# Kernel optimization log

Hardware: AMD Instinct MI355X
Metric: run time of the kernel (lower is better)

Reference implementation:

```python
import jax, jax.numpy as jnp
import numpy as np

N = 100000
E = 1600000
C_IN = 128
C_HID = 128


def setup_inputs() -> dict:
    key = jax.random.key(0)
    ks = jax.random.split(key, 6)
    x = jax.random.normal(ks[0], (N, C_IN), dtype=jnp.float32)
    edge_index = jax.random.randint(ks[1], (2, E), 0, N, dtype=jnp.int64)
    # GCNConv params: linear weight + bias per layer (glorot-ish scale)
    W1 = jax.random.normal(ks[2], (C_IN, C_HID), dtype=jnp.float32) / np.sqrt(C_IN)
    b1 = jnp.zeros((C_HID,), dtype=jnp.float32)
    W2 = jax.random.normal(ks[3], (C_HID, C_HID), dtype=jnp.float32) / np.sqrt(C_HID)
    b2 = jnp.zeros((C_HID,), dtype=jnp.float32)
    return {"x": x, "edge_index": edge_index, "W1": W1, "b1": b1, "W2": W2, "b2": b2}


def _gcn_conv(x, W, b, src, dst, n_nodes):
    # PyG GCNConv: h = D^{-1/2} (A + I) D^{-1/2} (x W) + b
    h = x @ W  # [N, C_out]
    # add self-loops
    loop = jnp.arange(n_nodes, dtype=src.dtype)
    s = jnp.concatenate([src, loop])
    d = jnp.concatenate([dst, loop])
    ones = jnp.ones(s.shape[0], dtype=h.dtype)
    deg = jax.ops.segment_sum(ones, d, num_segments=n_nodes)  # in-degree incl self-loop
    dinv = jnp.where(deg > 0, jax.lax.rsqrt(deg), 0.0)
    norm = dinv[s] * dinv[d]  # [E+N]
    msg = h[s] * norm[:, None]  # gather + scale
    out = jax.ops.segment_sum(msg, d, num_segments=n_nodes)  # scatter-add
    return out + b


def reference(x, edge_index, W1, b1, W2, b2):
    src, dst = edge_index[0], edge_index[1]
    h = jax.nn.relu(_gcn_conv(x, W1, b1, src, dst, N))
    h = jax.nn.relu(_gcn_conv(h, W2, b2, src, dst, N))
    return h
```

## Files before the change

kernel.cpp:

```cpp
#include <hip/hip_runtime.h>
#include <hip/hip_bf16.h>

#define GCN_N 100000
#define GB1 1563
#define NBUCK 391
#define BCAP 8192
#define KPWG 391

typedef unsigned short u16;
typedef unsigned int u32;
typedef float f32x4 __attribute__((ext_vector_type(4)));
typedef short bf16x8 __attribute__((ext_vector_type(8)));

union v16 { uint4 u; bf16x8 h; };

__device__ inline u16 f2bf(float f) {
    u32 u = __float_as_uint(f);
    return (u16)((u + 0x7fffu + ((u >> 16) & 1u)) >> 16);
}
__device__ inline u32 pack2(float a, float b) {
    return (u32)f2bf(a) | ((u32)f2bf(b) << 16);
}
__device__ inline float bf_lo(u32 u) { return __uint_as_float(u << 16); }
__device__ inline float bf_hi(u32 u) { return __uint_as_float(u & 0xffff0000u); }
__device__ inline u32 scale2(u32 p, float d) {
    return pack2(bf_lo(p) * d, bf_hi(p) * d);
}

__device__ inline void addu8(float* a, float4 v) {
    u32 u;
    u = __float_as_uint(v.x); a[0] += bf_lo(u); a[1] += bf_hi(u);
    u = __float_as_uint(v.y); a[2] += bf_lo(u); a[3] += bf_hi(u);
    u = __float_as_uint(v.z); a[4] += bf_lo(u); a[5] += bf_hi(u);
    u = __float_as_uint(v.w); a[6] += bf_lo(u); a[7] += bf_hi(u);
}
__device__ inline void setu8(float* a, float4 v) {
    u32 u;
    u = __float_as_uint(v.x); a[0] = bf_lo(u); a[1] = bf_hi(u);
    u = __float_as_uint(v.y); a[2] = bf_lo(u); a[3] = bf_hi(u);
    u = __float_as_uint(v.z); a[4] = bf_lo(u); a[5] = bf_hi(u);
    u = __float_as_uint(v.w); a[6] = bf_lo(u); a[7] = bf_hi(u);
}

__device__ inline void mfma16(f32x4& d, uint4 a, uint4 b) {
    v16 av, bv; av.u = a; bv.u = b;
    d = __builtin_amdgcn_mfma_f32_16x16x32_bf16(av.h, bv.h, d, 0, 0, 0);
}

__global__ __launch_bounds__(256) void k_init(int* __restrict__ gcursor,
                                              const float* __restrict__ W1,
                                              const float* __restrict__ W2,
                                              u16* __restrict__ Wt1,
                                              u16* __restrict__ Wt2) {
    if (blockIdx.x == 0) {
        for (int i = threadIdx.x; i < NBUCK; i += 256) gcursor[i] = 0;
        return;
    }
    const float* W = (blockIdx.x == 1) ? W1 : W2;
    u16* Wt = (blockIdx.x == 1) ? Wt1 : Wt2;
    for (int i = threadIdx.x; i < 16384; i += 256) {
        int k = i >> 7, nn = i & 127;
        Wt[nn * 128 + k] = f2bf(W[i]);
    }
}

template<int SCALE>
__device__ __attribute__((always_inline))
inline void gemm_core(const uint4* Xs, const u16* __restrict__ Wt,
                      const float* __restrict__ dinv, u16* __restrict__ H,
                      long long row0, int n) {
    const int t = threadIdx.x;
    const int wid = t >> 6;
    const int l = t & 63, lm = l & 15, lh = l >> 4;
    uint4 a[4];
    const int lrow = wid * 16 + lm;
    #pragma unroll
    for (int kk = 0; kk < 4; ++kk) {
        int byte = (lrow * 256 + kk * 64 + lh * 16) ^ ((lm & 7) << 4);
        a[kk] = Xs[byte >> 4];
    }
    const uint4* wb = (const uint4*)Wt;
    f32x4 acc[8];
    #pragma unroll
    for (int j = 0; j < 8; ++j) acc[j] = (f32x4){0.f, 0.f, 0.f, 0.f};
    #pragma unroll
    for (int j = 0; j < 8; ++j) {
        #pragma unroll
        for (int kk = 0; kk < 4; ++kk) {
            uint4 b = wb[(j * 16 + lm) * 16 + kk * 4 + lh];
            mfma16(acc[j], a[kk], b);
        }
    }
    long long gr0 = row0 + wid * 16 + lh * 4;
    float dv[4];
    #pragma unroll
    for (int r = 0; r < 4; ++r)
        dv[r] = SCALE ? ((gr0 + r < n) ? dinv[gr0 + r] : 0.f) : 1.f;
    #pragma unroll
    for (int j = 0; j < 8; ++j) {
        #pragma unroll
        for (int r = 0; r < 4; ++r) {
            long long grow = gr0 + r;
            if (grow < n)
                H[grow * 128 + j * 16 + lm] =
                    f2bf(SCALE ? acc[j][r] * dv[r] : acc[j][r]);
        }
    }
}

__global__ __launch_bounds__(256) void k_part_gemm1(
        const int* __restrict__ src, const int* __restrict__ dst,
        int* __restrict__ gcursor, u32* __restrict__ part,
        const float* __restrict__ X, const u16* __restrict__ Wt,
        u16* __restrict__ H, int E, int n) {
    __shared__ uint4 Xs[1024];
    if (blockIdx.x < KPWG) {
        int* lhist = (int*)Xs;
        int* lbase = lhist + NBUCK;
        int* lcur  = lbase + NBUCK;
        const int t = threadIdx.x;
        for (int i = t; i < NBUCK; i += 256) { lhist[i] = 0; lcur[i] = 0; }
        __syncthreads();
        const long long e0 = (long long)blockIdx.x * 4096;
        #pragma unroll
        for (int i = 0; i < 16; ++i) {
            long long e = e0 + i * 256 + t;
            if (e < E) atomicAdd(&lhist[dst[e] >> 8], 1);
        }
        __syncthreads();
        for (int i = t; i < NBUCK; i += 256) {
            int c = lhist[i];
            lbase[i] = c ? atomicAdd(&gcursor[i], c) : 0;
        }
        __syncthreads();
        #pragma unroll
        for (int i = 0; i < 16; ++i) {
            long long e = e0 + i * 256 + t;
            if (e < E) {
                int d = dst[e];
                int b = d >> 8;
                int ofs = lbase[b] + atomicAdd(&lcur[b], 1);
                if (ofs < BCAP)
                    part[(long long)b * BCAP + ofs] =
                        (u32)src[e] | ((u32)(d & 255) << 17);
            }
        }
        return;
    }
    const long long row0 = (long long)(blockIdx.x - KPWG) * 64;
    const int t = threadIdx.x;
    uint2* Xs2 = (uint2*)Xs;
    #pragma unroll
    for (int i = 0; i < 8; ++i) {
        int idx = i * 1024 + t * 4;
        int row = idx >> 7, k = idx & 127;
        long long grow = row0 + row; if (grow >= n) grow = n - 1;
        float4 v = *(const float4*)(X + grow * 128 + k);
        int byte = (row * 256 + k * 2) ^ ((row & 7) << 4);
        uint2 p; p.x = pack2(v.x, v.y); p.y = pack2(v.z, v.w);
        Xs2[byte >> 3] = p;
    }
    __syncthreads();
    gemm_core<0>(Xs, Wt, nullptr, H, row0, n);
}

__global__ __launch_bounds__(256) void k_csr(const int* __restrict__ gcursor,
                                             const u32* __restrict__ part,
                                             int* __restrict__ rowstart,
                                             float* __restrict__ dinv,
                                             int* __restrict__ csr,
                                             u16* __restrict__ h1, int n) {
    __shared__ int lcount[256];
    __shared__ int lpfx[256];
    __shared__ int lcur[256];
    __shared__ float ldinv[256];
    __shared__ int wpart[4];
    __shared__ int sbase;
    const int t = threadIdx.x;
    const int lane = t & 63, wid = t >> 6;
    const int b = blockIdx.x;
    int ps = ((t < b) ? min(gcursor[t], BCAP) : 0) +
             ((t + 256 < b) ? min(gcursor[t + 256], BCAP) : 0);
    #pragma unroll
    for (int off = 32; off > 0; off >>= 1) ps += __shfl_down(ps, off, 64);
    if (lane == 0) wpart[wid] = ps;
    lcount[t] = 0; lcur[t] = 0;
    __syncthreads();
    if (t == 0) sbase = wpart[0] + wpart[1] + wpart[2] + wpart[3];
    __syncthreads();
    const int base = sbase;
    const int cnt = min(gcursor[b], BCAP);
    const u32* bp = part + (long long)b * BCAP;
    for (int i = t; i < cnt; i += 256) atomicAdd(&lcount[bp[i] >> 17], 1);
    __syncthreads();
    if (t == 0) {
        int run = 0;
        #pragma unroll 8
        for (int j = 0; j < 256; ++j) { lpfx[j] = run; run += lcount[j]; }
    }
    __syncthreads();
    int node = b * 256 + t;
    {
        float dv = rsqrtf((float)(lcount[t] + 1));
        ldinv[t] = dv;
        if (node < n) {
            rowstart[node] = base + lpfx[t];
            dinv[node] = dv;
        }
    }
    if (b == NBUCK - 1 && t == 0) rowstart[n] = base + cnt;
    __syncthreads();
    for (int i = t; i < cnt; i += 256) {
        u32 v = bp[i];
        int loc = v >> 17;
        int p = base + lpfx[loc] + atomicAdd(&lcur[loc], 1);
        csr[p] = (int)(v & 0x1FFFFu);
    }
    uint4* h4 = (uint4*)h1;
    const long long rbase = (long long)b * 256;
    for (int i = t; i < 4096; i += 256) {
        int loc = i >> 4;
        long long nd = rbase + loc;
        if (nd < n) {
            float d = ldinv[loc];
            long long gi = nd * 16 + (i & 15);
            uint4 v = h4[gi];
            v.x = scale2(v.x, d); v.y = scale2(v.y, d);
            v.z = scale2(v.z, d); v.w = scale2(v.w, d);
            h4[gi] = v;
        }
    }
}

__global__ __launch_bounds__(256) void k_gemm2(
        const u16* __restrict__ X, const u16* __restrict__ Wt,
        const float* __restrict__ dinv, u16* __restrict__ H, int n) {
    __shared__ uint4 Xs[1024];
    const long long row0 = (long long)blockIdx.x * 64;
    const int t = threadIdx.x;
    #pragma unroll
    for (int i = 0; i < 4; ++i) {
        int idx = i * 2048 + t * 8;
        int row = idx >> 7, k = idx & 127;
        long long grow = row0 + row; if (grow >= n) grow = n - 1;
        uint4 v = *(const uint4*)(X + grow * 128 + k);
        int byte = (row * 256 + k * 2) ^ ((row & 7) << 4);
        Xs[byte >> 4] = v;
    }
    __syncthreads();
    gemm_core<1>(Xs, Wt, dinv, H, row0, n);
}

template<int OUT_BF16>
__global__ __launch_bounds__(256) void k_agg(const u16* __restrict__ h,
                                             const int* __restrict__ rowstart,
                                             const int* __restrict__ csr_src,
                                             const float* __restrict__ dinv,
                                             const float* __restrict__ bias,
                                             void* __restrict__ outp, int n) {
    const int q    = threadIdx.x >> 4;
    const int sub  = threadIdx.x & 15;
    const int node = blockIdx.x * 16 + q;
    if (node >= n) return;
    const float di = dinv[node];
    int e = rowstart[node];
    const int end = rowstart[node + 1];
    const float4* __restrict__ hv = (const float4*)h;
    float a[8], b[8];
    setu8(a, hv[(size_t)node * 16 + sub]);
    #pragma unroll
    for (int j = 0; j < 8; ++j) b[j] = 0.f;
    for (; e + 8 <= end; e += 8) {
        int s0 = csr_src[e + 0], s1 = csr_src[e + 1];
        int s2 = csr_src[e + 2], s3 = csr_src[e + 3];
        int s4 = csr_src[e + 4], s5 = csr_src[e + 5];
        int s6 = csr_src[e + 6], s7 = csr_src[e + 7];
        float4 v0 = hv[(size_t)s0 * 16 + sub];
        float4 v1 = hv[(size_t)s1 * 16 + sub];
        float4 v2 = hv[(size_t)s2 * 16 + sub];
        float4 v3 = hv[(size_t)s3 * 16 + sub];
        float4 v4 = hv[(size_t)s4 * 16 + sub];
        float4 v5 = hv[(size_t)s5 * 16 + sub];
        float4 v6 = hv[(size_t)s6 * 16 + sub];
        float4 v7 = hv[(size_t)s7 * 16 + sub];
        addu8(a, v0); addu8(b, v1); addu8(a, v2); addu8(b, v3);
        addu8(a, v4); addu8(b, v5); addu8(a, v6); addu8(b, v7);
    }
    for (; e + 4 <= end; e += 4) {
        int s0 = csr_src[e + 0], s1 = csr_src[e + 1];
        int s2 = csr_src[e + 2], s3 = csr_src[e + 3];
        float4 v0 = hv[(size_t)s0 * 16 + sub];
        float4 v1 = hv[(size_t)s1 * 16 + sub];
        float4 v2 = hv[(size_t)s2 * 16 + sub];
        float4 v3 = hv[(size_t)s3 * 16 + sub];
        addu8(a, v0); addu8(b, v1); addu8(a, v2); addu8(b, v3);
    }
    for (; e < end; ++e) {
        float4 v = hv[(size_t)csr_src[e] * 16 + sub];
        addu8(a, v);
    }
    const float4 bv0 = ((const float4*)bias)[sub * 2];
    const float4 bv1 = ((const float4*)bias)[sub * 2 + 1];
    float o[8];
    o[0] = fmaxf(fmaf(a[0] + b[0], di, bv0.x), 0.f);
    o[1] = fmaxf(fmaf(a[1] + b[1], di, bv0.y), 0.f);
    o[2] = fmaxf(fmaf(a[2] + b[2], di, bv0.z), 0.f);
    o[3] = fmaxf(fmaf(a[3] + b[3], di, bv0.w), 0.f);
    o[4] = fmaxf(fmaf(a[4] + b[4], di, bv1.x), 0.f);
    o[5] = fmaxf(fmaf(a[5] + b[5], di, bv1.y), 0.f);
    o[6] = fmaxf(fmaf(a[6] + b[6], di, bv1.z), 0.f);
    o[7] = fmaxf(fmaf(a[7] + b[7], di, bv1.w), 0.f);
    if (OUT_BF16) {
        float4 pv;
        pv.x = __uint_as_float(pack2(o[0], o[1]));
        pv.y = __uint_as_float(pack2(o[2], o[3]));
        pv.z = __uint_as_float(pack2(o[4], o[5]));
        pv.w = __uint_as_float(pack2(o[6], o[7]));
        ((float4*)outp)[(size_t)node * 16 + sub] = pv;
    } else {
        float* out = (float*)outp + (size_t)node * 128 + sub * 8;
        float4 w0 = {o[0], o[1], o[2], o[3]};
        float4 w1 = {o[4], o[5], o[6], o[7]};
        *(float4*)(out + 0) = w0;
        *(float4*)(out + 4) = w1;
    }
}


extern "C" void kernel_launch(void* const* d_in, const int* in_sizes, int n_in,
                              void* d_out, int out_size, void* d_ws, size_t ws_size,
                              hipStream_t stream) {
    const float* x   = (const float*)d_in[0];
    const int* edges = (const int*)d_in[1];
    const float* W1  = (const float*)d_in[2];
    const float* b1  = (const float*)d_in[3];
    const float* W2  = (const float*)d_in[4];
    const float* b2  = (const float*)d_in[5];
    const int E = in_sizes[1] / 2;
    const int N = GCN_N;
    const int* srcp = edges;
    const int* dstp = edges + E;

    char* ws = (char*)d_ws;
    int*   gcursor  = (int*)(ws + 0);
    int*   rowstart = (int*)(ws + 4096);
    float* dinvp    = (float*)(ws + 413696);
    u16*   wt1      = (u16*)(ws + 819200);
    u16*   wt2      = (u16*)(ws + 851968);
    u32*   part     = (u32*)(ws + 1048576);
    int*   csr      = (int*)(ws + 14680064);
    u16*   h1       = (u16*)(ws + 23068672);
    u16*   h2       = (u16*)(ws + 50331648);

    k_init<<<3, 256, 0, stream>>>(gcursor, W1, W2, wt1, wt2);
    k_part_gemm1<<<KPWG + GB1, 256, 0, stream>>>(srcp, dstp, gcursor, part,
                                                 x, wt1, h1, E, N);
    k_csr<<<NBUCK, 256, 0, stream>>>(gcursor, part, rowstart, dinvp, csr, h1, N);
    k_agg<1><<<(N + 15) / 16, 256, 0, stream>>>(h1, rowstart, csr, dinvp, b1, h2, N);
    k_gemm2<<<GB1, 256, 0, stream>>>(h2, wt2, dinvp, h1, N);
    k_agg<0><<<(N + 15) / 16, 256, 0, stream>>>(h1, rowstart, csr, dinvp, b2, d_out, N);
}
```

Before: 264.3 us.

## Replace global-cursor bucket partition with per-workgroup sorted fragments and offset table

The partition kernel now sorts each workgroup's 4096 edges locally by bucket and writes them contiguously, recording per-bucket offsets in a u16 table, instead of reserving space per bucket with global atomics into fixed-capacity bins. The CSR kernel gathers each bucket's runs from all 391 fragments using that table. This removes the BCAP overflow truncation and the contention on global cursors, and shrinks the workspace. In exchange, the CSR kernel does many short serial per-thread loops over run fragments, which can load-balance poorly and make reads less coalesced.

```diff
diff --git a/kernel.cpp b/kernel.cpp
--- a/kernel.cpp
+++ b/kernel.cpp
@@ -4,7 +4,6 @@
 #define GCN_N 100000
 #define GB1 1563
 #define NBUCK 391
-#define BCAP 8192
 #define KPWG 391
 
 typedef unsigned short u16;
@@ -47,13 +46,13 @@
     d = __builtin_amdgcn_mfma_f32_16x16x32_bf16(av.h, bv.h, d, 0, 0, 0);
 }
 
-__global__ __launch_bounds__(256) void k_init(int* __restrict__ gcursor,
+__global__ __launch_bounds__(256) void k_init(int* __restrict__ gtotal,
                                               const float* __restrict__ W1,
                                               const float* __restrict__ W2,
                                               u16* __restrict__ Wt1,
                                               u16* __restrict__ Wt2) {
     if (blockIdx.x == 0) {
-        for (int i = threadIdx.x; i < NBUCK; i += 256) gcursor[i] = 0;
+        for (int i = threadIdx.x; i < NBUCK; i += 256) gtotal[i] = 0;
         return;
     }
     const float* W = (blockIdx.x == 1) ? W1 : W2;
@@ -110,39 +109,47 @@
 
 __global__ __launch_bounds__(256) void k_part_gemm1(
         const int* __restrict__ src, const int* __restrict__ dst,
-        int* __restrict__ gcursor, u32* __restrict__ part,
+        int* __restrict__ gtotal, u32* __restrict__ part_edges,
+        u16* __restrict__ frag_off,
         const float* __restrict__ X, const u16* __restrict__ Wt,
         u16* __restrict__ H, int E, int n) {
     __shared__ uint4 Xs[1024];
     if (blockIdx.x < KPWG) {
-        int* lhist = (int*)Xs;
-        int* lbase = lhist + NBUCK;
-        int* lcur  = lbase + NBUCK;
+        int* loff = (int*)Xs;
+        int* lcur = loff + 392;
         const int t = threadIdx.x;
-        for (int i = t; i < NBUCK; i += 256) { lhist[i] = 0; lcur[i] = 0; }
+        for (int i = t; i < 392; i += 256) loff[i] = 0;
+        for (int i = t; i < 391; i += 256) lcur[i] = 0;
         __syncthreads();
         const long long e0 = (long long)blockIdx.x * 4096;
+        const int ecnt = (int)min(4096LL, (long long)E - e0);
         #pragma unroll
         for (int i = 0; i < 16; ++i) {
-            long long e = e0 + i * 256 + t;
-            if (e < E) atomicAdd(&lhist[dst[e] >> 8], 1);
+            int idx = i * 256 + t;
+            if (idx < ecnt) atomicAdd(&loff[dst[e0 + idx] >> 8], 1);
         }
         __syncthreads();
-        for (int i = t; i < NBUCK; i += 256) {
-            int c = lhist[i];
-            lbase[i] = c ? atomicAdd(&gcursor[i], c) : 0;
+        if (t == 0) {
+            int run = 0;
+            for (int j = 0; j < 391; ++j) { int c = loff[j]; loff[j] = run; run += c; }
+            loff[391] = run;
         }
         __syncthreads();
+        for (int i = t; i < 392; i += 256)
+            frag_off[blockIdx.x * 392 + i] = (u16)loff[i];
+        for (int i = t; i < 391; i += 256) {
+            int c = loff[i + 1] - loff[i];
+            if (c) atomicAdd(&gtotal[i], c);
+        }
+        u32* frag = part_edges + (long long)blockIdx.x * 4096;
         #pragma unroll
         for (int i = 0; i < 16; ++i) {
-            long long e = e0 + i * 256 + t;
-            if (e < E) {
-                int d = dst[e];
+            int idx = i * 256 + t;
+            if (idx < ecnt) {
+                int d = dst[e0 + idx];
                 int b = d >> 8;
-                int ofs = lbase[b] + atomicAdd(&lcur[b], 1);
-                if (ofs < BCAP)
-                    part[(long long)b * BCAP + ofs] =
-                        (u32)src[e] | ((u32)(d & 255) << 17);
+                int pos = loff[b] + atomicAdd(&lcur[b], 1);
+                frag[pos] = (u32)src[e0 + idx] | ((u32)(d & 255) << 17);
             }
         }
         return;
@@ -164,12 +171,15 @@
     gemm_core<0>(Xs, Wt, nullptr, H, row0, n);
 }
 
-__global__ __launch_bounds__(256) void k_csr(const int* __restrict__ gcursor,
-                                             const u32* __restrict__ part,
+__global__ __launch_bounds__(256) void k_csr(const int* __restrict__ gtotal,
+                                             const u32* __restrict__ part_edges,
+                                             const u16* __restrict__ frag_off,
                                              int* __restrict__ rowstart,
                                              float* __restrict__ dinv,
                                              int* __restrict__ csr,
                                              u16* __restrict__ h1, int n) {
+    __shared__ int runstart[391];
+    __shared__ int runlen[391];
     __shared__ int lcount[256];
     __shared__ int lpfx[256];
     __shared__ int lcur[256];
@@ -179,19 +189,27 @@
     const int t = threadIdx.x;
     const int lane = t & 63, wid = t >> 6;
     const int b = blockIdx.x;
-    int ps = ((t < b) ? min(gcursor[t], BCAP) : 0) +
-             ((t + 256 < b) ? min(gcursor[t + 256], BCAP) : 0);
+    int ps = ((t < b) ? gtotal[t] : 0) + ((t + 256 < b) ? gtotal[t + 256] : 0);
     #pragma unroll
     for (int off = 32; off > 0; off >>= 1) ps += __shfl_down(ps, off, 64);
     if (lane == 0) wpart[wid] = ps;
     lcount[t] = 0; lcur[t] = 0;
+    for (int w = t; w < 391; w += 256) {
+        int s  = frag_off[w * 392 + b];
+        int e2 = frag_off[w * 392 + b + 1];
+        runstart[w] = w * 4096 + s;
+        runlen[w] = e2 - s;
+    }
     __syncthreads();
     if (t == 0) sbase = wpart[0] + wpart[1] + wpart[2] + wpart[3];
     __syncthreads();
     const int base = sbase;
-    const int cnt = min(gcursor[b], BCAP);
-    const u32* bp = part + (long long)b * BCAP;
-    for (int i = t; i < cnt; i += 256) atomicAdd(&lcount[bp[i] >> 17], 1);
+    const int cnt = gtotal[b];
+    for (int w = t; w < 391; w += 256) {
+        const u32* rp = part_edges + runstart[w];
+        int len = runlen[w];
+        for (int i = 0; i < len; ++i) atomicAdd(&lcount[rp[i] >> 17], 1);
+    }
     __syncthreads();
     if (t == 0) {
         int run = 0;
@@ -210,11 +228,15 @@
     }
     if (b == NBUCK - 1 && t == 0) rowstart[n] = base + cnt;
     __syncthreads();
-    for (int i = t; i < cnt; i += 256) {
-        u32 v = bp[i];
-        int loc = v >> 17;
-        int p = base + lpfx[loc] + atomicAdd(&lcur[loc], 1);
-        csr[p] = (int)(v & 0x1FFFFu);
+    for (int w = t; w < 391; w += 256) {
+        const u32* rp = part_edges + runstart[w];
+        int len = runlen[w];
+        for (int i = 0; i < len; ++i) {
+            u32 v = rp[i];
+            int loc = v >> 17;
+            int p = base + lpfx[loc] + atomicAdd(&lcur[loc], 1);
+            csr[p] = (int)(v & 0x1FFFFu);
+        }
     }
     uint4* h4 = (uint4*)h1;
     const long long rbase = (long long)b * 256;
@@ -342,20 +364,22 @@
     const int* dstp = edges + E;
 
     char* ws = (char*)d_ws;
-    int*   gcursor  = (int*)(ws + 0);
+    int*   gtotal   = (int*)(ws + 0);
     int*   rowstart = (int*)(ws + 4096);
     float* dinvp    = (float*)(ws + 413696);
     u16*   wt1      = (u16*)(ws + 819200);
     u16*   wt2      = (u16*)(ws + 851968);
-    u32*   part     = (u32*)(ws + 1048576);
-    int*   csr      = (int*)(ws + 14680064);
-    u16*   h1       = (u16*)(ws + 23068672);
+    u16*   frag_off = (u16*)(ws + 917504);
+    u32*   part     = (u32*)(ws + 1310720);
+    int*   csr      = (int*)(ws + 8388608);
+    u16*   h1       = (u16*)(ws + 16777216);
     u16*   h2       = (u16*)(ws + 50331648);
 
-    k_init<<<3, 256, 0, stream>>>(gcursor, W1, W2, wt1, wt2);
-    k_part_gemm1<<<KPWG + GB1, 256, 0, stream>>>(srcp, dstp, gcursor, part,
-                                                 x, wt1, h1, E, N);
-    k_csr<<<NBUCK, 256, 0, stream>>>(gcursor, part, rowstart, dinvp, csr, h1, N);
+    k_init<<<3, 256, 0, stream>>>(gtotal, W1, W2, wt1, wt2);
+    k_part_gemm1<<<KPWG + GB1, 256, 0, stream>>>(srcp, dstp, gtotal, part,
+                                                 frag_off, x, wt1, h1, E, N);
+    k_csr<<<NBUCK, 256, 0, stream>>>(gtotal, part, frag_off, rowstart, dinvp,
+                                     csr, h1, N);
     k_agg<1><<<(N + 15) / 16, 256, 0, stream>>>(h1, rowstart, csr, dinvp, b1, h2, N);
     k_gemm2<<<GB1, 256, 0, stream>>>(h2, wt2, dinvp, h1, N);
     k_agg<0><<<(N + 15) / 16, 256, 0, stream>>>(h1, rowstart, csr, dinvp, b2, d_out, N);
```

After: 274.0 us. +3.7%, slower.
